# Kernel tuning notes

Measured on AMD Instinct MI355X. Metric: run time of the kernel, lower is better.

## Reference

```python
import jax, jax.numpy as jnp
import numpy as np

# Poincare ball, curvature c = 1. Assumed manifold ops (standard hyperbolic-attention
# formulations, matching the hypll-style API used by the module):
#   HLinear(x)                ~ expmap0(logmap0(x) @ W + b)   (tangent-space linear)
#   attention_similarity      ~ (-d_poincare(q,k))/tau + gamma
#   attention_activation      ~ softmax over keys
#   attention_midpoint        ~ Mobius gyromidpoint: 0.5 (x) [sum_k w lam(v) v / sum_k w (lam(v)-1)]
#   cat                       ~ expmap0(concat(logmap0(heads)))

EPS = 1e-6
MAX_TANH_ARG = 1.0 - 1e-5

def _norm(x):
    return jnp.sqrt(jnp.clip(jnp.sum(x * x, axis=-1, keepdims=True), EPS))

def expmap0(v):
    n = _norm(v)
    return jnp.tanh(n) * v / n

def logmap0(x):
    n = _norm(x)
    return jnp.arctanh(jnp.minimum(n, MAX_TANH_ARG)) * x / n

def hlinear(x, W, b):
    return expmap0(logmap0(x) @ W + b)

def pairwise_poincare_dist(q, k):
    # q: [B,H,Sq,D] on ball, k: [B,Sk,D] on ball -> d: [B,H,Sq,Sk]
    qn = jnp.clip(jnp.sum(q * q, axis=-1), 0.0, 1.0 - 1e-5)            # [B,H,Sq]
    kn = jnp.clip(jnp.sum(k * k, axis=-1), 0.0, 1.0 - 1e-5)            # [B,Sk]
    dot = jnp.einsum('bhqd,bkd->bhqk', q, k)                            # GEMM-like
    sq = jnp.clip(qn[..., :, None] + kn[:, None, None, :] - 2.0 * dot, 0.0)
    denom = jnp.clip((1.0 - qn)[..., :, None] * (1.0 - kn)[:, None, None, :], EPS)
    arg = 1.0 + 2.0 * sq / denom
    return jnp.arccosh(jnp.maximum(arg, 1.0 + 1e-7))

def mobius_scalar_mul(r, x):
    n = _norm(x)
    return jnp.tanh(r * jnp.arctanh(jnp.minimum(n, MAX_TANH_ARG))) * x / n


def reference(query, key, value, Wq, bq, Wk, bk, Wv, bv, Wo, bo, scale_tau, scale_gamma):
    # batch_first=True; query/key/value: [B,S,D] points on the Poincare ball
    B, S, D = query.shape
    H = Wq.shape[0]

    # per-head full-dimension query projections, vectorized over heads
    tq = logmap0(query)                                                 # [B,S,D]
    q_h = expmap0(jnp.einsum('bsd,hde->bhse', tq, Wq) + bq[None, :, None, :])  # [B,H,S,D]
    # shared K/V projections (use_separate_kv_per_head=False -> MQA)
    k = hlinear(key, Wk, bk)                                            # [B,S,D]
    v = hlinear(value, Wv, bv)                                          # [B,S,D]

    tau = jnp.exp(-scale_tau[0])          # module passes tau = 1/exp(scale_tau)
    gamma = scale_gamma[0]

    d = pairwise_poincare_dist(q_h, k)                                  # [B,H,Sq,Sk]
    sim = -d / tau + gamma
    w = jax.nn.softmax(sim, axis=-1)                                    # [B,H,Sq,Sk]

    # Mobius gyromidpoint of values, weighted per query
    vn = jnp.clip(jnp.sum(v * v, axis=-1), 0.0, 1.0 - 1e-5)             # [B,Sk]
    lam = 2.0 / (1.0 - vn)                                              # [B,Sk]
    num = jnp.einsum('bhqk,bk,bkd->bhqd', w, lam, v)                    # [B,H,Sq,D]
    den = jnp.einsum('bhqk,bk->bhq', w, lam - 1.0)[..., None]           # [B,H,Sq,1]
    mid = mobius_scalar_mul(0.5, num / jnp.clip(den, EPS))              # [B,H,Sq,D]

    # manifold.cat: tangent-space concat of heads, back to the ball
    t = logmap0(mid)                                                    # [B,H,S,D]
    t = jnp.transpose(t, (0, 2, 1, 3)).reshape(B, S, H * D)             # [B,S,H*D]
    concat = expmap0(t)
    return hlinear(concat, Wo, bo)                                      # [B,S,D]


def setup_inputs() -> dict:
    key0 = jax.random.key(0)
    ks = jax.random.split(key0, 16)
    B, S, D, H = 4, 1024, 512, 8
    proj = lambda k: expmap0(0.02 * jax.random.normal(k, (B, S, D), dtype=jnp.float32))
    w_init = lambda k, shape, fan_in: (jax.random.normal(k, shape, dtype=jnp.float32) / np.sqrt(fan_in)).astype(jnp.float32)
    return {
        'query': proj(ks[0]),
        'key': proj(ks[1]),
        'value': proj(ks[2]),
        'Wq': w_init(ks[3], (H, D, D), D),
        'bq': 0.01 * jax.random.normal(ks[4], (H, D), dtype=jnp.float32),
        'Wk': w_init(ks[5], (D, D), D),
        'bk': 0.01 * jax.random.normal(ks[6], (D,), dtype=jnp.float32),
        'Wv': w_init(ks[7], (D, D), D),
        'bv': 0.01 * jax.random.normal(ks[8], (D,), dtype=jnp.float32),
        'Wo': w_init(ks[9], (H * D, D), H * D),
        'bo': 0.01 * jax.random.normal(ks[10], (D,), dtype=jnp.float32),
        'scale_tau': jnp.zeros((1,), dtype=jnp.float32),
        'scale_gamma': jnp.zeros((1,), dtype=jnp.float32),
    }
```

## Files before the change

### kernel.cpp

```cpp
#include <hip/hip_runtime.h>
#include <math.h>

constexpr int B_ = 4, S_ = 1024, D_ = 512, H_ = 8;
constexpr float EPS_ = 1e-6f;
constexpr float MAXT = 1.0f - 1e-5f;

typedef __attribute__((ext_vector_type(8))) short bf16x8;
typedef __attribute__((ext_vector_type(4))) float f32x4;

__device__ __forceinline__ ushort f2b(float f) {
    unsigned u = __float_as_uint(f);
    unsigned r = u + 0x7fffu + ((u >> 16) & 1u);
    return (ushort)(r >> 16);
}
__device__ __forceinline__ float b2f(ushort h) {
    return __uint_as_float(((unsigned)h) << 16);
}

__device__ __forceinline__ void async16(const ushort* g, ushort* l) {
    __builtin_amdgcn_global_load_lds(
        (const __attribute__((address_space(1))) unsigned int*)g,
        (__attribute__((address_space(3))) unsigned int*)l, 16, 0, 0);
}

__device__ __forceinline__ float blk_reduce_sum(float v, float* sm) {
    for (int o = 32; o > 0; o >>= 1) v += __shfl_down(v, o, 64);
    int lane = threadIdx.x & 63, wid = threadIdx.x >> 6;
    if (lane == 0) sm[wid] = v;
    __syncthreads();
    if (threadIdx.x == 0) sm[0] = sm[0] + sm[1] + sm[2] + sm[3];
    __syncthreads();
    float r = sm[0];
    __syncthreads();
    return r;
}

constexpr int GC_ABUF = 256 * 32;
constexpr int GC_BUF = (256 + 128) * 32;
constexpr int GC_SH = GC_BUF * 2;

__device__ __forceinline__ void gemm_core256(const ushort* __restrict__ A,
                                             const ushort* __restrict__ B,
                                             int lda, int ldb, int K, int m0, int n0,
                                             ushort* __restrict__ sh, f32x4 acc[4][8]) {
    const int tid = threadIdx.x;
    const int w = tid >> 6, lane = tid & 63;
    const int quad = lane >> 4, lx = lane & 15;
    const int rr = lane >> 2, c = lane & 3;

    const ushort* aP[4];
    int aOff[4];
#pragma unroll
    for (int i = 0; i < 4; i++) {
        int r = w * 64 + i * 16 + rr;
        int q = c ^ ((r >> 1) & 3);
        aP[i] = A + (size_t)(m0 + r) * lda + q * 8;
        aOff[i] = (w * 64 + i * 16) * 32;
    }
    const ushort* bP[2];
    int bOff[2];
#pragma unroll
    for (int i = 0; i < 2; i++) {
        int r = w * 32 + i * 16 + rr;
        int q = c ^ ((r >> 1) & 3);
        bP[i] = B + (size_t)(n0 + r) * ldb + q * 8;
        bOff[i] = GC_ABUF + (w * 32 + i * 16) * 32;
    }

    int raOff[4], rbOff[8];
#pragma unroll
    for (int i = 0; i < 4; i++) {
        int ra = w * 64 + i * 16 + lx;
        raOff[i] = ra * 32 + (quad ^ ((ra >> 1) & 3)) * 8;
    }
#pragma unroll
    for (int j = 0; j < 8; j++) {
        int rb = j * 16 + lx;
        rbOff[j] = GC_ABUF + rb * 32 + (quad ^ ((rb >> 1) & 3)) * 8;
    }
#pragma unroll
    for (int i = 0; i < 4; i++)
#pragma unroll
        for (int j = 0; j < 8; j++) acc[i][j] = (f32x4)(0.0f);

#pragma unroll
    for (int i = 0; i < 4; i++) async16(aP[i], sh + aOff[i]);
#pragma unroll
    for (int i = 0; i < 2; i++) async16(bP[i], sh + bOff[i]);

    const int nsteps = K >> 5;
    for (int s = 0; s < nsteps; s++) {
        ushort* cur = sh + (s & 1) * GC_BUF;
        if (s + 1 < nsteps) {
            ushort* nxt = sh + ((s + 1) & 1) * GC_BUF;
            int k0 = (s + 1) << 5;
#pragma unroll
            for (int i = 0; i < 4; i++) async16(aP[i] + k0, nxt + aOff[i]);
#pragma unroll
            for (int i = 0; i < 2; i++) async16(bP[i] + k0, nxt + bOff[i]);
            asm volatile("s_waitcnt vmcnt(6)" ::: "memory");
        } else {
            asm volatile("s_waitcnt vmcnt(0)" ::: "memory");
        }
        asm volatile("s_barrier" ::: "memory");
        bf16x8 af[4], bfr[8];
#pragma unroll
        for (int i = 0; i < 4; i++) af[i] = *(const bf16x8*)(cur + raOff[i]);
#pragma unroll
        for (int j = 0; j < 8; j++) bfr[j] = *(const bf16x8*)(cur + rbOff[j]);
#pragma unroll
        for (int i = 0; i < 4; i++)
#pragma unroll
            for (int j = 0; j < 8; j++)
                acc[i][j] = __builtin_amdgcn_mfma_f32_16x16x32_bf16(af[i], bfr[j], acc[i][j], 0, 0, 0);
        asm volatile("s_waitcnt lgkmcnt(0)" ::: "memory");
        asm volatile("s_barrier" ::: "memory");
    }
}

__global__ __launch_bounds__(256, 2) void k_gemm_proj_all(const ushort* __restrict__ tq,
                                                          const ushort* __restrict__ tk,
                                                          const ushort* __restrict__ tv,
                                                          const ushort* __restrict__ WqT,
                                                          const ushort* __restrict__ WkT,
                                                          const ushort* __restrict__ WvT,
                                                          const float* __restrict__ bq,
                                                          const float* __restrict__ bk,
                                                          const float* __restrict__ bv,
                                                          ushort* __restrict__ yq,
                                                          ushort* __restrict__ yk,
                                                          ushort* __restrict__ yv,
                                                          float* __restrict__ ssq,
                                                          float* __restrict__ ssk,
                                                          float* __restrict__ ssv) {
    __shared__ ushort sh[GC_SH];
    int z = blockIdx.z;
    const ushort* A;
    const ushort* BT;
    const float* bias;
    ushort* C;
    float* SS;
    int remap = 0, h = 0;
    if (z == 0) { A = tk; BT = WkT; bias = bk; C = yk; SS = ssk; }
    else if (z == 1) { A = tv; BT = WvT; bias = bv; C = yv; SS = ssv; }
    else {
        h = z - 2;
        A = tq; BT = WqT + (size_t)h * 512 * 512; bias = bq + (size_t)h * 512;
        C = yq; SS = ssq; remap = 1;
    }
    f32x4 acc[4][8];
    int m0 = blockIdx.y * 256, n0 = blockIdx.x * 128;
    gemm_core256(A, BT, 512, 512, 512, m0, n0, sh, acc);
    int tid = threadIdx.x, w = tid >> 6, lane = tid & 63;
    int quad = lane >> 4, lx = lane & 15;
#pragma unroll
    for (int i = 0; i < 4; i++)
#pragma unroll
        for (int reg = 0; reg < 4; reg++) {
            int m = m0 + w * 64 + i * 16 + quad * 4 + reg;
            size_t orow = remap ? (size_t)((m >> 10) * H_ + h) * S_ + (m & 1023) : (size_t)m;
            float ssum = 0.0f;
#pragma unroll
            for (int j = 0; j < 8; j++) {
                int n = n0 + j * 16 + lx;
                ushort hb = f2b(acc[i][j][reg] + bias[n]);
                C[orow * 512 + n] = hb;
                float yv_ = b2f(hb);
                ssum += yv_ * yv_;
            }
            for (int o = 8; o; o >>= 1) ssum += __shfl_xor(ssum, o, 64);
            if (lx == 0) atomicAdd(&SS[orow], ssum);
        }
}

__global__ __launch_bounds__(256) void k_ballfactors(const float* __restrict__ ssq,
                                                     const float* __restrict__ ssk,
                                                     const float* __restrict__ ssv,
                                                     float* __restrict__ fq,
                                                     float* __restrict__ qn2,
                                                     float* __restrict__ fk,
                                                     float* __restrict__ kn2,
                                                     float* __restrict__ cv,
                                                     float* __restrict__ dsc) {
    int idx = blockIdx.x * 256 + threadIdx.x;
    if (idx >= 40960) return;
    float ss;
    if (idx < 32768) ss = ssq[idx];
    else if (idx < 36864) ss = ssk[idx - 32768];
    else ss = ssv[idx - 36864];
    float n = sqrtf(fmaxf(ss, EPS_));
    float f = tanhf(n) / n;
    float bn2 = fminf(f * f * ss, MAXT);
    if (idx < 32768) {
        fq[idx] = f;
        qn2[idx] = bn2;
    } else if (idx < 36864) {
        fk[idx - 32768] = f;
        kn2[idx - 32768] = bn2;
    } else {
        int r = idx - 36864;
        float lam = 2.0f / (1.0f - bn2);
        float c = f * lam;
        cv[r] = c;
        dsc[r] = (lam - 1.0f) / c;
    }
}

__global__ __launch_bounds__(256, 2) void k_gemm_score(const ushort* __restrict__ Yq,
                                                       const ushort* __restrict__ Yk,
                                                       ushort* __restrict__ E,
                                                       float* __restrict__ den,
                                                       const float* __restrict__ fq,
                                                       const float* __restrict__ qn2,
                                                       const float* __restrict__ fk,
                                                       const float* __restrict__ kn2,
                                                       const float* __restrict__ cv,
                                                       const float* __restrict__ dsc,
                                                       const float* __restrict__ stau) {
    __shared__ ushort sh[GC_SH];
    int b = blockIdx.z;
    int m0 = blockIdx.y * 256, n0 = blockIdx.x * 128;
    const ushort* Aq = Yq + (size_t)b * 8192 * 512;
    const ushort* Bk = Yk + (size_t)b * 1024 * 512;
    E += (size_t)b * 8192 * 1024;
    den += (size_t)b * 8192;
    const float* fqb = fq + (size_t)b * 8192;
    const float* qn2b = qn2 + (size_t)b * 8192;
    const float* fkb = fk + (size_t)b * 1024;
    const float* kn2b = kn2 + (size_t)b * 1024;
    const float* cvb = cv + (size_t)b * 1024;
    const float* dscb = dsc + (size_t)b * 1024;

    f32x4 acc[4][8];
    gemm_core256(Aq, Bk, 512, 512, 512, m0, n0, sh, acc);
    float itau = expf(stau[0]);
    bool tau1 = (itau == 1.0f);
    int tid = threadIdx.x, w_ = tid >> 6, lane = tid & 63;
    int quad = lane >> 4, lx = lane & 15;
    float fkv[8], kn2v[8], cvv[8], dscv[8], rk[8];
#pragma unroll
    for (int j = 0; j < 8; j++) {
        int n = n0 + j * 16 + lx;
        fkv[j] = fkb[n];
        kn2v[j] = kn2b[n];
        rk[j] = __builtin_amdgcn_rcpf(1.0f - kn2v[j]);
        cvv[j] = cvb[n];
        dscv[j] = dscb[n];
    }
#pragma unroll
    for (int i = 0; i < 4; i++)
#pragma unroll
        for (int reg = 0; reg < 4; reg++) {
            int m = m0 + w_ * 64 + i * 16 + quad * 4 + reg;
            float fqm = fqb[m];
            float q = qn2b[m];
            float rq2 = 2.0f * __builtin_amdgcn_rcpf(1.0f - q);
            float rsum = 0.0f;
#pragma unroll
            for (int j = 0; j < 8; j++) {
                float dot = fqm * fkv[j] * acc[i][j][reg];
                float sq = fmaxf(q + kn2v[j] - 2.0f * dot, 0.0f);
                float rr2 = fminf(rq2 * rk[j], 2e6f);
                float w = fmaxf(sq * rr2, 1e-7f);
                float root = __builtin_amdgcn_sqrtf(__builtin_fmaf(w, w, 2.0f * w));
                float t = 1.0f + w + root;
                float e = tau1 ? __builtin_amdgcn_rcpf(t)
                               : __builtin_amdgcn_exp2f(-itau * __builtin_amdgcn_logf(t));
                ushort eb = f2b(e * cvv[j]);
                int n = n0 + j * 16 + lx;
                E[(size_t)m * 1024 + n] = eb;
                rsum += b2f(eb) * dscv[j];
            }
            for (int o = 8; o; o >>= 1) rsum += __shfl_xor(rsum, o, 64);
            if (lx == 0) atomicAdd(&den[m], rsum);
        }
}

__global__ __launch_bounds__(256, 2) void k_gemm_attnv(const ushort* __restrict__ E,
                                                       const ushort* __restrict__ VT,
                                                       const float* __restrict__ den,
                                                       ushort* __restrict__ Ub,
                                                       float* __restrict__ ssU) {
    __shared__ ushort sh[GC_SH];
    int b = blockIdx.z;
    int m0 = blockIdx.y * 256, n0 = blockIdx.x * 128;
    E += (size_t)b * 8192 * 1024;
    VT += (size_t)b * 512 * 1024;
    den += (size_t)b * 8192;
    Ub += (size_t)b * 8192 * 512;
    ssU += (size_t)b * 8192;
    f32x4 acc[4][8];
    gemm_core256(E, VT, 1024, 1024, 1024, m0, n0, sh, acc);
    int tid = threadIdx.x, w = tid >> 6, lane = tid & 63;
    int quad = lane >> 4, lx = lane & 15;
#pragma unroll
    for (int i = 0; i < 4; i++)
#pragma unroll
        for (int reg = 0; reg < 4; reg++) {
            int m = m0 + w * 64 + i * 16 + quad * 4 + reg;
            float inv = __builtin_amdgcn_rcpf(fmaxf(den[m], EPS_));
            float ssum = 0.0f;
#pragma unroll
            for (int j = 0; j < 8; j++) {
                int n = n0 + j * 16 + lx;
                float u = acc[i][j][reg] * inv;
                Ub[(size_t)m * 512 + n] = f2b(u);
                ssum += u * u;
            }
            for (int o = 8; o; o >>= 1) ssum += __shfl_xor(ssum, o, 64);
            if (lx == 0) atomicAdd(&ssU[m], ssum);
        }
}

__global__ __launch_bounds__(256, 2) void k_gemm_sk(const ushort* __restrict__ Ub,
                                                    const ushort* __restrict__ WoT,
                                                    float* __restrict__ Cp) {
    __shared__ ushort sh[GC_SH];
    int z = blockIdx.z;
    int m0 = blockIdx.y * 256, n0 = blockIdx.x * 128;
    int bb = m0 >> 10, s0 = m0 & 1023;
    const ushort* A = Ub + ((size_t)(bb * H_ + z) * S_ + s0) * 512;
    const ushort* BT = WoT + (size_t)z * 512;
    float* C = Cp + (size_t)z * 4096 * 512;
    f32x4 acc[4][8];
    gemm_core256(A, BT, 512, 4096, 512, 0, n0, sh, acc);
    int tid = threadIdx.x, w = tid >> 6, lane = tid & 63;
    int quad = lane >> 4, lx = lane & 15;
#pragma unroll
    for (int i = 0; i < 4; i++)
#pragma unroll
        for (int reg = 0; reg < 4; reg++) {
            int m = m0 + w * 64 + i * 16 + quad * 4 + reg;
#pragma unroll
            for (int j = 0; j < 8; j++) {
                int n = n0 + j * 16 + lx;
                C[(size_t)m * 512 + n] = acc[i][j][reg];
            }
        }
}

__global__ __launch_bounds__(256) void k_hyperfactors(const float* __restrict__ ssU,
                                                      float* __restrict__ Asc8) {
    int idx = blockIdx.x * 256 + threadIdx.x;
    if (idx >= B_ * S_) return;
    int b = idx >> 10, s = idx & 1023;
    float f12[8];
    float sum = 0.0f;
#pragma unroll
    for (int h = 0; h < H_; h++) {
        float ss = ssU[(size_t)(b * H_ + h) * S_ + s];
        float n = sqrtf(fmaxf(ss, EPS_));
        float a = 0.5f * atanhf(fminf(n, MAXT));
        float f1 = tanhf(a) / n;
        float mss = f1 * f1 * ss;
        float nm = sqrtf(fmaxf(mss, EPS_));
        float f2 = atanhf(fminf(nm, MAXT)) / nm;
        f12[h] = f1 * f2;
        sum += f12[h] * f12[h] * ss;
    }
    float nc = sqrtf(fmaxf(sum, EPS_));
    float f3 = tanhf(nc) / nc;
    float css = f3 * f3 * sum;
    float nc2 = sqrtf(fmaxf(css, EPS_));
    float f4 = atanhf(fminf(nc2, MAXT)) / nc2;
    float g = f3 * f4;
#pragma unroll
    for (int h = 0; h < H_; h++) Asc8[(size_t)idx * 8 + h] = f12[h] * g;
}

__global__ __launch_bounds__(256) void k_final_reduce_expmap(const float* __restrict__ Cp,
                                                             const float* __restrict__ Asc8,
                                                             const float* __restrict__ bo,
                                                             float* __restrict__ out) {
    __shared__ float sm[8];
    int r = blockIdx.x;
    float a[8];
#pragma unroll
    for (int z = 0; z < 8; z++) a[z] = Asc8[(size_t)r * 8 + z];
    float v0 = bo[threadIdx.x], v1 = bo[threadIdx.x + 256];
#pragma unroll
    for (int z = 0; z < 8; z++) {
        const float* row = Cp + ((size_t)z * 4096 + r) * 512;
        v0 += a[z] * row[threadIdx.x];
        v1 += a[z] * row[threadIdx.x + 256];
    }
    float ss = blk_reduce_sum(v0 * v0 + v1 * v1, sm);
    float n = sqrtf(fmaxf(ss, EPS_));
    float f = tanhf(n) / n;
    float* o = out + (size_t)r * D_;
    o[threadIdx.x] = f * v0;
    o[threadIdx.x + 256] = f * v1;
}

__global__ __launch_bounds__(256) void k_logmap_bf16(const float* __restrict__ q,
                                                     const float* __restrict__ k,
                                                     const float* __restrict__ v,
                                                     ushort* __restrict__ tq,
                                                     ushort* __restrict__ tk,
                                                     ushort* __restrict__ tv) {
    __shared__ float sm[8];
    const float* x = (blockIdx.y == 0) ? q : (blockIdx.y == 1) ? k : v;
    ushort* t = (blockIdx.y == 0) ? tq : (blockIdx.y == 1) ? tk : tv;
    int r = blockIdx.x;
    const float* xr = x + (size_t)r * D_;
    float v0 = xr[threadIdx.x], v1 = xr[threadIdx.x + 256];
    float ss = blk_reduce_sum(v0 * v0 + v1 * v1, sm);
    float n = sqrtf(fmaxf(ss, EPS_));
    float f = atanhf(fminf(n, MAXT)) / n;
    ushort* tr = t + (size_t)r * D_;
    tr[threadIdx.x] = f2b(f * v0);
    tr[threadIdx.x + 256] = f2b(f * v1);
}

__global__ __launch_bounds__(256) void k_transpose_sqw(const float* __restrict__ Wk,
                                                       const float* __restrict__ Wv,
                                                       const float* __restrict__ Wq,
                                                       ushort* __restrict__ WkT,
                                                       ushort* __restrict__ WvT,
                                                       ushort* __restrict__ WqT) {
    __shared__ float t[32][33];
    int z = blockIdx.z;
    const float* in;
    ushort* out;
    if (z == 0) { in = Wk; out = WkT; }
    else if (z == 1) { in = Wv; out = WvT; }
    else { in = Wq + (size_t)(z - 2) * 512 * 512; out = WqT + (size_t)(z - 2) * 512 * 512; }
    int c0 = blockIdx.x * 32, r0 = blockIdx.y * 32;
    int tx = threadIdx.x & 31, ty = threadIdx.x >> 5;
    for (int rr = ty; rr < 32; rr += 8) t[rr][tx] = in[(size_t)(r0 + rr) * 512 + c0 + tx];
    __syncthreads();
    for (int rr = ty; rr < 32; rr += 8)
        out[(size_t)(c0 + rr) * 512 + r0 + tx] = f2b(t[tx][rr]);
}

__global__ __launch_bounds__(256) void k_transpose_f2b(const float* __restrict__ in,
                                                       ushort* __restrict__ out, int R, int C) {
    __shared__ float t[32][33];
    int c0 = blockIdx.x * 32, r0 = blockIdx.y * 32;
    int tx = threadIdx.x & 31, ty = threadIdx.x >> 5;
    for (int rr = ty; rr < 32; rr += 8) t[rr][tx] = in[(size_t)(r0 + rr) * C + c0 + tx];
    __syncthreads();
    for (int rr = ty; rr < 32; rr += 8)
        out[(size_t)(c0 + rr) * R + r0 + tx] = f2b(t[tx][rr]);
}

__global__ __launch_bounds__(256) void k_transpose_b2b(const ushort* __restrict__ in,
                                                       ushort* __restrict__ out, int R, int C,
                                                       size_t zin, size_t zout) {
    __shared__ ushort t[32][34];
    in += (size_t)blockIdx.z * zin;
    out += (size_t)blockIdx.z * zout;
    int c0 = blockIdx.x * 32, r0 = blockIdx.y * 32;
    int tx = threadIdx.x & 31, ty = threadIdx.x >> 5;
    for (int rr = ty; rr < 32; rr += 8) t[rr][tx] = in[(size_t)(r0 + rr) * C + c0 + tx];
    __syncthreads();
    for (int rr = ty; rr < 32; rr += 8)
        out[(size_t)(c0 + rr) * R + r0 + tx] = t[tx][rr];
}

extern "C" void kernel_launch(void* const* d_in, const int* in_sizes, int n_in,
                              void* d_out, int out_size, void* d_ws, size_t ws_size,
                              hipStream_t stream) {
    (void)in_sizes; (void)n_in; (void)out_size; (void)ws_size;
    const float* query = (const float*)d_in[0];
    const float* key = (const float*)d_in[1];
    const float* value = (const float*)d_in[2];
    const float* Wq = (const float*)d_in[3];
    const float* bq = (const float*)d_in[4];
    const float* Wk = (const float*)d_in[5];
    const float* bk = (const float*)d_in[6];
    const float* Wv = (const float*)d_in[7];
    const float* bv = (const float*)d_in[8];
    const float* Wo = (const float*)d_in[9];
    const float* bo = (const float*)d_in[10];
    const float* stau = (const float*)d_in[11];
    float* out = (float*)d_out;

    char* p = (char*)d_ws;
    auto alloc = [&](size_t bytes) {
        char* r = p;
        p += (bytes + 255) & ~(size_t)255;
        return r;
    };
    ushort* tq = (ushort*)alloc((size_t)4096 * 512 * 2);
    ushort* tk = (ushort*)alloc((size_t)4096 * 512 * 2);
    ushort* tv = (ushort*)alloc((size_t)4096 * 512 * 2);
    ushort* WqT = (ushort*)alloc((size_t)8 * 512 * 512 * 2);
    ushort* WkT = (ushort*)alloc((size_t)512 * 512 * 2);
    ushort* WvT = (ushort*)alloc((size_t)512 * 512 * 2);
    ushort* WoT = (ushort*)alloc((size_t)4096 * 512 * 2);
    ushort* yq = (ushort*)alloc((size_t)32768 * 512 * 2);
    ushort* yk = (ushort*)alloc((size_t)4096 * 512 * 2);
    ushort* yv = (ushort*)alloc((size_t)4096 * 512 * 2);
    ushort* yvT = (ushort*)alloc((size_t)4 * 512 * 1024 * 2);
    ushort* Ub = (ushort*)alloc((size_t)32768 * 512 * 2);
    ushort* Sc = (ushort*)alloc((size_t)4 * 8192 * 1024 * 2);
    float* den = (float*)alloc(32768 * 4);
    float* ssU = (float*)alloc(32768 * 4);
    float* ssq = (float*)alloc(32768 * 4);
    float* ssk = (float*)alloc(4096 * 4);
    float* ssv = (float*)alloc(4096 * 4);
    float* fq = (float*)alloc(32768 * 4);
    float* qn2 = (float*)alloc(32768 * 4);
    float* fk = (float*)alloc(4096 * 4);
    float* kn2 = (float*)alloc(4096 * 4);
    float* cv = (float*)alloc(4096 * 4);
    float* dsc = (float*)alloc(4096 * 4);
    float* Asc8 = (float*)alloc(32768 * 4);
    float* Cp = (float*)Sc;

    hipMemsetAsync(den, 0, (size_t)(32768 * 3 + 4096 * 2 + 192) * 4, stream);

    k_logmap_bf16<<<dim3(4096, 3), 256, 0, stream>>>(query, key, value, tq, tk, tv);

    k_transpose_sqw<<<dim3(16, 16, 10), 256, 0, stream>>>(Wk, Wv, Wq, WkT, WvT, WqT);
    k_transpose_f2b<<<dim3(16, 128, 1), 256, 0, stream>>>(Wo, WoT, 4096, 512);

    k_gemm_proj_all<<<dim3(4, 16, 10), 256, 0, stream>>>(tq, tk, tv, WqT, WkT, WvT, bq, bk, bv,
                                                         yq, yk, yv, ssq, ssk, ssv);

    k_ballfactors<<<160, 256, 0, stream>>>(ssq, ssk, ssv, fq, qn2, fk, kn2, cv, dsc);
    k_transpose_b2b<<<dim3(16, 32, 4), 256, 0, stream>>>(yv, yvT, 1024, 512,
                                                         (size_t)1024 * 512, (size_t)512 * 1024);

    k_gemm_score<<<dim3(8, 32, 4), 256, 0, stream>>>(yq, yk, Sc, den, fq, qn2, fk, kn2, cv, dsc,
                                                     stau);
    k_gemm_attnv<<<dim3(4, 32, 4), 256, 0, stream>>>(Sc, yvT, den, Ub, ssU);

    k_hyperfactors<<<16, 256, 0, stream>>>(ssU, Asc8);

    k_gemm_sk<<<dim3(4, 16, 8), 256, 0, stream>>>(Ub, WoT, Cp);
    k_final_reduce_expmap<<<4096, 256, 0, stream>>>(Cp, Asc8, bo, out);
}
```

Measured before the change: 361.5 us.

## Triple-buffer GEMM core and merge small kernels to cut launch count

The shared GEMM core moves from double to triple buffering of LDS tiles, prefetching two k-steps ahead with adjusted vmcnt waits to hide more global-load latency. Several small kernels are merged: the four weight transposes become one launch, the ball-factor computation and the V transpose share one launch, and the per-row hyperbolic factors are computed inline inside the final reduce kernel. This removes launch overhead and an intermediate buffer. The extra LDS per block may lower occupancy for the GEMM kernels.

```diff
diff --git a/kernel.cpp b/kernel.cpp
--- a/kernel.cpp
+++ b/kernel.cpp
@@ -37,7 +37,7 @@
 
 constexpr int GC_ABUF = 256 * 32;
 constexpr int GC_BUF = (256 + 128) * 32;
-constexpr int GC_SH = GC_BUF * 2;
+constexpr int GC_SH = GC_BUF * 3;
 
 __device__ __forceinline__ void gemm_core256(const ushort* __restrict__ A,
                                              const ushort* __restrict__ B,
@@ -83,21 +83,30 @@
 #pragma unroll
         for (int j = 0; j < 8; j++) acc[i][j] = (f32x4)(0.0f);
 
+    const int nsteps = K >> 5;
 #pragma unroll
     for (int i = 0; i < 4; i++) async16(aP[i], sh + aOff[i]);
 #pragma unroll
     for (int i = 0; i < 2; i++) async16(bP[i], sh + bOff[i]);
-
-    const int nsteps = K >> 5;
+#pragma unroll
+    for (int i = 0; i < 4; i++) async16(aP[i] + 32, sh + GC_BUF + aOff[i]);
+#pragma unroll
+    for (int i = 0; i < 2; i++) async16(bP[i] + 32, sh + GC_BUF + bOff[i]);
+
+    int bufid = 0;
     for (int s = 0; s < nsteps; s++) {
-        ushort* cur = sh + (s & 1) * GC_BUF;
-        if (s + 1 < nsteps) {
-            ushort* nxt = sh + ((s + 1) & 1) * GC_BUF;
-            int k0 = (s + 1) << 5;
+        ushort* cur = sh + bufid * GC_BUF;
+        if (s + 2 < nsteps) {
+            int nb = bufid + 2;
+            if (nb >= 3) nb -= 3;
+            ushort* nxt = sh + nb * GC_BUF;
+            int k0 = (s + 2) << 5;
 #pragma unroll
             for (int i = 0; i < 4; i++) async16(aP[i] + k0, nxt + aOff[i]);
 #pragma unroll
             for (int i = 0; i < 2; i++) async16(bP[i] + k0, nxt + bOff[i]);
+            asm volatile("s_waitcnt vmcnt(12)" ::: "memory");
+        } else if (s + 1 < nsteps) {
             asm volatile("s_waitcnt vmcnt(6)" ::: "memory");
         } else {
             asm volatile("s_waitcnt vmcnt(0)" ::: "memory");
@@ -115,6 +124,7 @@
                 acc[i][j] = __builtin_amdgcn_mfma_f32_16x16x32_bf16(af[i], bfr[j], acc[i][j], 0, 0, 0);
         asm volatile("s_waitcnt lgkmcnt(0)" ::: "memory");
         asm volatile("s_barrier" ::: "memory");
+        bufid = (bufid == 2) ? 0 : bufid + 1;
     }
 }
 
@@ -173,16 +183,33 @@
         }
 }
 
-__global__ __launch_bounds__(256) void k_ballfactors(const float* __restrict__ ssq,
-                                                     const float* __restrict__ ssk,
-                                                     const float* __restrict__ ssv,
-                                                     float* __restrict__ fq,
-                                                     float* __restrict__ qn2,
-                                                     float* __restrict__ fk,
-                                                     float* __restrict__ kn2,
-                                                     float* __restrict__ cv,
-                                                     float* __restrict__ dsc) {
-    int idx = blockIdx.x * 256 + threadIdx.x;
+__global__ __launch_bounds__(256) void k_post_proj(const ushort* __restrict__ yv,
+                                                   ushort* __restrict__ yvT,
+                                                   const float* __restrict__ ssq,
+                                                   const float* __restrict__ ssk,
+                                                   const float* __restrict__ ssv,
+                                                   float* __restrict__ fq,
+                                                   float* __restrict__ qn2,
+                                                   float* __restrict__ fk,
+                                                   float* __restrict__ kn2,
+                                                   float* __restrict__ cv,
+                                                   float* __restrict__ dsc) {
+    int lin = blockIdx.x;
+    if (lin < 2048) {
+        __shared__ ushort t[32][34];
+        int z = lin >> 9, rem = lin & 511;
+        int by = rem >> 4, bx = rem & 15;
+        const ushort* in = yv + (size_t)z * 1024 * 512;
+        ushort* out = yvT + (size_t)z * 512 * 1024;
+        int c0 = bx * 32, r0 = by * 32;
+        int tx = threadIdx.x & 31, ty = threadIdx.x >> 5;
+        for (int rr = ty; rr < 32; rr += 8) t[rr][tx] = in[(size_t)(r0 + rr) * 512 + c0 + tx];
+        __syncthreads();
+        for (int rr = ty; rr < 32; rr += 8)
+            out[(size_t)(c0 + rr) * 1024 + r0 + tx] = t[tx][rr];
+        return;
+    }
+    int idx = (lin - 2048) * 256 + threadIdx.x;
     if (idx >= 40960) return;
     float ss;
     if (idx < 32768) ss = ssq[idx];
@@ -339,15 +366,15 @@
         }
 }
 
-__global__ __launch_bounds__(256) void k_hyperfactors(const float* __restrict__ ssU,
-                                                      float* __restrict__ Asc8) {
-    int idx = blockIdx.x * 256 + threadIdx.x;
-    if (idx >= B_ * S_) return;
-    int b = idx >> 10, s = idx & 1023;
-    float f12[8];
-    float sum = 0.0f;
-#pragma unroll
-    for (int h = 0; h < H_; h++) {
+__global__ __launch_bounds__(256) void k_final_reduce_expmap(const float* __restrict__ Cp,
+                                                             const float* __restrict__ ssU,
+                                                             const float* __restrict__ bo,
+                                                             float* __restrict__ out) {
+    __shared__ float sm[24];
+    int r = blockIdx.x;
+    int b = r >> 10, s = r & 1023;
+    if (threadIdx.x < 8) {
+        int h = threadIdx.x;
         float ss = ssU[(size_t)(b * H_ + h) * S_ + s];
         float n = sqrtf(fmaxf(ss, EPS_));
         float a = 0.5f * atanhf(fminf(n, MAXT));
@@ -355,36 +382,35 @@
         float mss = f1 * f1 * ss;
         float nm = sqrtf(fmaxf(mss, EPS_));
         float f2 = atanhf(fminf(nm, MAXT)) / nm;
-        f12[h] = f1 * f2;
-        sum += f12[h] * f12[h] * ss;
-    }
-    float nc = sqrtf(fmaxf(sum, EPS_));
-    float f3 = tanhf(nc) / nc;
-    float css = f3 * f3 * sum;
-    float nc2 = sqrtf(fmaxf(css, EPS_));
-    float f4 = atanhf(fminf(nc2, MAXT)) / nc2;
-    float g = f3 * f4;
-#pragma unroll
-    for (int h = 0; h < H_; h++) Asc8[(size_t)idx * 8 + h] = f12[h] * g;
-}
-
-__global__ __launch_bounds__(256) void k_final_reduce_expmap(const float* __restrict__ Cp,
-                                                             const float* __restrict__ Asc8,
-                                                             const float* __restrict__ bo,
-                                                             float* __restrict__ out) {
-    __shared__ float sm[8];
-    int r = blockIdx.x;
-    float a[8];
-#pragma unroll
-    for (int z = 0; z < 8; z++) a[z] = Asc8[(size_t)r * 8 + z];
+        float f12 = f1 * f2;
+        sm[h] = f12;
+        sm[8 + h] = f12 * f12 * ss;
+    }
+    __syncthreads();
+    if (threadIdx.x == 0) {
+        float sum = 0.0f;
+#pragma unroll
+        for (int h = 0; h < 8; h++) sum += sm[8 + h];
+        float nc = sqrtf(fmaxf(sum, EPS_));
+        float f3 = tanhf(nc) / nc;
+        float css = f3 * f3 * sum;
+        float nc2 = sqrtf(fmaxf(css, EPS_));
+        float f4 = atanhf(fminf(nc2, MAXT)) / nc2;
+        sm[16] = f3 * f4;
+    }
+    __syncthreads();
+    float g = sm[16];
+    float a8[8];
+#pragma unroll
+    for (int z = 0; z < 8; z++) a8[z] = sm[z] * g;
     float v0 = bo[threadIdx.x], v1 = bo[threadIdx.x + 256];
 #pragma unroll
     for (int z = 0; z < 8; z++) {
         const float* row = Cp + ((size_t)z * 4096 + r) * 512;
-        v0 += a[z] * row[threadIdx.x];
-        v1 += a[z] * row[threadIdx.x + 256];
-    }
-    float ss = blk_reduce_sum(v0 * v0 + v1 * v1, sm);
+        v0 += a8[z] * row[threadIdx.x];
+        v1 += a8[z] * row[threadIdx.x + 256];
+    }
+    float ss = blk_reduce_sum(v0 * v0 + v1 * v1, sm + 17);
     float n = sqrtf(fmaxf(ss, EPS_));
     float f = tanhf(n) / n;
     float* o = out + (size_t)r * D_;
@@ -412,50 +438,36 @@
     tr[threadIdx.x + 256] = f2b(f * v1);
 }
 
-__global__ __launch_bounds__(256) void k_transpose_sqw(const float* __restrict__ Wk,
+__global__ __launch_bounds__(256) void k_transpose_all(const float* __restrict__ Wk,
                                                        const float* __restrict__ Wv,
                                                        const float* __restrict__ Wq,
+                                                       const float* __restrict__ Wo,
                                                        ushort* __restrict__ WkT,
                                                        ushort* __restrict__ WvT,
-                                                       ushort* __restrict__ WqT) {
+                                                       ushort* __restrict__ WqT,
+                                                       ushort* __restrict__ WoT) {
     __shared__ float t[32][33];
     int z = blockIdx.z;
-    const float* in;
-    ushort* out;
-    if (z == 0) { in = Wk; out = WkT; }
-    else if (z == 1) { in = Wv; out = WvT; }
-    else { in = Wq + (size_t)(z - 2) * 512 * 512; out = WqT + (size_t)(z - 2) * 512 * 512; }
     int c0 = blockIdx.x * 32, r0 = blockIdx.y * 32;
     int tx = threadIdx.x & 31, ty = threadIdx.x >> 5;
-    for (int rr = ty; rr < 32; rr += 8) t[rr][tx] = in[(size_t)(r0 + rr) * 512 + c0 + tx];
-    __syncthreads();
-    for (int rr = ty; rr < 32; rr += 8)
-        out[(size_t)(c0 + rr) * 512 + r0 + tx] = f2b(t[tx][rr]);
-}
-
-__global__ __launch_bounds__(256) void k_transpose_f2b(const float* __restrict__ in,
-                                                       ushort* __restrict__ out, int R, int C) {
-    __shared__ float t[32][33];
-    int c0 = blockIdx.x * 32, r0 = blockIdx.y * 32;
-    int tx = threadIdx.x & 31, ty = threadIdx.x >> 5;
-    for (int rr = ty; rr < 32; rr += 8) t[rr][tx] = in[(size_t)(r0 + rr) * C + c0 + tx];
-    __syncthreads();
-    for (int rr = ty; rr < 32; rr += 8)
-        out[(size_t)(c0 + rr) * R + r0 + tx] = f2b(t[tx][rr]);
-}
-
-__global__ __launch_bounds__(256) void k_transpose_b2b(const ushort* __restrict__ in,
-                                                       ushort* __restrict__ out, int R, int C,
-                                                       size_t zin, size_t zout) {
-    __shared__ ushort t[32][34];
-    in += (size_t)blockIdx.z * zin;
-    out += (size_t)blockIdx.z * zout;
-    int c0 = blockIdx.x * 32, r0 = blockIdx.y * 32;
-    int tx = threadIdx.x & 31, ty = threadIdx.x >> 5;
-    for (int rr = ty; rr < 32; rr += 8) t[rr][tx] = in[(size_t)(r0 + rr) * C + c0 + tx];
-    __syncthreads();
-    for (int rr = ty; rr < 32; rr += 8)
-        out[(size_t)(c0 + rr) * R + r0 + tx] = t[tx][rr];
+    if (z < 10) {
+        const float* in;
+        ushort* out;
+        if (z == 0) { in = Wk; out = WkT; }
+        else if (z == 1) { in = Wv; out = WvT; }
+        else { in = Wq + (size_t)(z - 2) * 512 * 512; out = WqT + (size_t)(z - 2) * 512 * 512; }
+        for (int rr = ty; rr < 32; rr += 8) t[rr][tx] = in[(size_t)(r0 + rr) * 512 + c0 + tx];
+        __syncthreads();
+        for (int rr = ty; rr < 32; rr += 8)
+            out[(size_t)(c0 + rr) * 512 + r0 + tx] = f2b(t[tx][rr]);
+    } else {
+        int zz = z - 10;
+        const float* in = Wo + (size_t)zz * 512 * 512;
+        for (int rr = ty; rr < 32; rr += 8) t[rr][tx] = in[(size_t)(r0 + rr) * 512 + c0 + tx];
+        __syncthreads();
+        for (int rr = ty; rr < 32; rr += 8)
+            WoT[(size_t)(c0 + rr) * 4096 + zz * 512 + r0 + tx] = f2b(t[tx][rr]);
+    }
 }
 
 extern "C" void kernel_launch(void* const* d_in, const int* in_sizes, int n_in,
@@ -506,29 +518,23 @@
     float* kn2 = (float*)alloc(4096 * 4);
     float* cv = (float*)alloc(4096 * 4);
     float* dsc = (float*)alloc(4096 * 4);
-    float* Asc8 = (float*)alloc(32768 * 4);
     float* Cp = (float*)Sc;
 
     hipMemsetAsync(den, 0, (size_t)(32768 * 3 + 4096 * 2 + 192) * 4, stream);
 
     k_logmap_bf16<<<dim3(4096, 3), 256, 0, stream>>>(query, key, value, tq, tk, tv);
 
-    k_transpose_sqw<<<dim3(16, 16, 10), 256, 0, stream>>>(Wk, Wv, Wq, WkT, WvT, WqT);
-    k_transpose_f2b<<<dim3(16, 128, 1), 256, 0, stream>>>(Wo, WoT, 4096, 512);
+    k_transpose_all<<<dim3(16, 16, 18), 256, 0, stream>>>(Wk, Wv, Wq, Wo, WkT, WvT, WqT, WoT);
 
     k_gemm_proj_all<<<dim3(4, 16, 10), 256, 0, stream>>>(tq, tk, tv, WqT, WkT, WvT, bq, bk, bv,
                                                          yq, yk, yv, ssq, ssk, ssv);
 
-    k_ballfactors<<<160, 256, 0, stream>>>(ssq, ssk, ssv, fq, qn2, fk, kn2, cv, dsc);
-    k_transpose_b2b<<<dim3(16, 32, 4), 256, 0, stream>>>(yv, yvT, 1024, 512,
-                                                         (size_t)1024 * 512, (size_t)512 * 1024);
+    k_post_proj<<<2208, 256, 0, stream>>>(yv, yvT, ssq, ssk, ssv, fq, qn2, fk, kn2, cv, dsc);
 
     k_gemm_score<<<dim3(8, 32, 4), 256, 0, stream>>>(yq, yk, Sc, den, fq, qn2, fk, kn2, cv, dsc,
                                                      stau);
     k_gemm_attnv<<<dim3(4, 32, 4), 256, 0, stream>>>(Sc, yvT, den, Ub, ssU);
 
-    k_hyperfactors<<<16, 256, 0, stream>>>(ssU, Asc8);
-
     k_gemm_sk<<<dim3(4, 16, 8), 256, 0, stream>>>(Ub, WoT, Cp);
-    k_final_reduce_expmap<<<4096, 256, 0, stream>>>(Cp, Asc8, bo, out);
-}
+    k_final_reduce_expmap<<<4096, 256, 0, stream>>>(Cp, ssU, bo, out);
+}
```

After: 353.5 us. 2.2% less time.
